# Optimization experiments

Measured on AMD Instinct MI355X. Metric: run time of the kernel, lower is better.

The kernel has to match this reference:

```python
import jax, jax.numpy as jnp
import numpy as np

BS, L, DIM = 16, 2048, 512
NUM_GROUPS, NUM_CODES = 2, 320
CODE_DIM = 256
VAR_DIM = CODE_DIM // NUM_GROUPS  # 128
INNER = DIM * 2                    # projFactor=2
TAU = 2.0                          # max(maxTemp*decay**0, minTemp) at numUpdates=0


def setup_inputs() -> dict:
    key = jax.random.key(0)
    ks = jax.random.split(key, 7)
    x = jax.random.normal(ks[0], (BS, L, DIM), jnp.float32)
    # gumbels = -log(Exp(1)) == standard Gumbel noise, matching torch's exponential_().log().neg()
    gumbels = jax.random.gumbel(ks[1], (BS * L * NUM_GROUPS, NUM_CODES), jnp.float32)
    W1 = jax.random.normal(ks[2], (DIM, INNER), jnp.float32) * (1.0 / np.sqrt(DIM))
    b1 = jnp.zeros((INNER,), jnp.float32)
    W2 = jax.random.normal(ks[3], (INNER, NUM_GROUPS * NUM_CODES), jnp.float32) * (1.0 / np.sqrt(INNER))
    b2 = jnp.zeros((NUM_GROUPS * NUM_CODES,), jnp.float32)
    # nn.init.uniform_ on embeddings: U[0,1); combineGroups=True -> single shared codebook (numCodes, varDim)
    emb = jax.random.uniform(ks[4], (NUM_CODES, VAR_DIM), jnp.float32)
    return {"x": x, "gumbels": gumbels, "W1": W1, "b1": b1, "W2": W2, "b2": b2, "emb": emb}


def reference(x, gumbels, W1, b1, W2, b2, emb):
    bs, l, d = x.shape
    xt = x.reshape(bs * l, d)
    h = jax.nn.gelu(xt @ W1 + b1, approximate=False)          # (N, INNER), torch GELU is exact erf
    logits = (h @ W2 + b2).reshape(bs * l * NUM_GROUPS, NUM_CODES)
    # training path: gumbel-softmax with straight-through hard one-hot
    soft = jax.nn.softmax((logits + gumbels) / TAU, axis=-1)  # (N*G, C)
    idx = jnp.argmax(soft, axis=-1)
    hard = jax.nn.one_hot(idx, NUM_CODES, dtype=soft.dtype)
    st = hard + soft - jax.lax.stop_gradient(soft)            # straight-through estimator
    st = st.reshape(bs * l, NUM_GROUPS, NUM_CODES)
    # combineGroups=True: embeddings repeated per group == shared codebook; the
    # (broadcast-mul).sum(-2) in torch is exactly this contraction (no huge intermediate).
    out = jnp.einsum('ngc,cd->ngd', st, emb)                  # (N, G, varDim)
    return out.reshape(bs, l, NUM_GROUPS * VAR_DIM)
```

## Files before the change

### kernel.cpp

```cpp
#include <hip/hip_runtime.h>
#include <math.h>


#define NTOK   32768
#define DIM    512
#define INNER  1024
#define NC     320
#define NGRP   2
#define VD     128
#define OUTD   256
#define RCAP   2048
#define MARGIN 8.0e-3f

#define L_LIST 16u
#define L_W1T  (64u<<10)
#define L_W2T  (2u<<20)
#define L_XH   (4u<<20)
#define L_H    (36u<<20)
#define L_PART (100u<<20)
#define L_HDW  (104u<<20)
#define WS_NEED (120u<<20)

#define W1F_OFF (1u<<20)
#define W2F_OFF (1u<<21)
#define SMEM_BYTES (65536 + 3328)

typedef _Float16 half8 __attribute__((ext_vector_type(8)));
typedef _Float16 half4 __attribute__((ext_vector_type(4)));
typedef float    f32x4 __attribute__((ext_vector_type(4)));

__device__ __forceinline__ float gelu_f(float s) {
  return 0.5f * s * (1.0f + erff(s * 0.70710678118654752440f));
}

#if defined(__has_builtin) && __has_builtin(__builtin_amdgcn_global_load_lds)
#define GLOAD16(gp, ldsbase, lane) \
  __builtin_amdgcn_global_load_lds((const __attribute__((address_space(1))) void*)(gp), \
                                   (__attribute__((address_space(3))) void*)(ldsbase), 16, 0, 0)
#else
#define GLOAD16(gp, ldsbase, lane) \
  do { *(uint4*)((char*)(ldsbase) + (lane) * 16) = *(const uint4*)(gp); } while (0)
#endif

#define XH_JOBS   2097152
#define W1T_JOBS  65536
#define W2T_JOBS  81920
#define PREP_JOBS (XH_JOBS + W1T_JOBS + W2T_JOBS)
__global__ __launch_bounds__(256)
void prep2_kernel(const float* __restrict__ x, const float* __restrict__ W1,
                  const float* __restrict__ W2, _Float16* __restrict__ xh,
                  _Float16* __restrict__ W1T, _Float16* __restrict__ W2T,
                  unsigned* __restrict__ cnt) {
  const int o = blockIdx.x * 256 + threadIdx.x;
  if (o == 0) cnt[0] = 0u;
  if (o < XH_JOBS) {
    const float4 v0 = *(const float4*)(x + (size_t)o * 8);
    const float4 v1 = *(const float4*)(x + (size_t)o * 8 + 4);
    half8 hv;
    hv[0] = (_Float16)v0.x; hv[1] = (_Float16)v0.y; hv[2] = (_Float16)v0.z; hv[3] = (_Float16)v0.w;
    hv[4] = (_Float16)v1.x; hv[5] = (_Float16)v1.y; hv[6] = (_Float16)v1.z; hv[7] = (_Float16)v1.w;
    *(half8*)(xh + (size_t)o * 8) = hv;
  } else if (o < XH_JOBS + W1T_JOBS) {
    const int q = o - XH_JOBS;
    const int i = q >> 6, k0 = (q & 63) * 8;
#pragma unroll
    for (int j = 0; j < 8; ++j)
      W1T[(size_t)i * DIM + k0 + j] = (_Float16)W1[(size_t)(k0 + j) * INNER + i];
  } else if (o < PREP_JOBS) {
    const int q = o - XH_JOBS - W1T_JOBS;
    const int c = q >> 7, i0 = (q & 127) * 8;
#pragma unroll
    for (int j = 0; j < 8; ++j)
      W2T[(size_t)c * INNER + i0 + j] = (_Float16)W2[(size_t)(i0 + j) * (NC * NGRP) + c];
  }
}

__global__ __launch_bounds__(256, 4)
void gemm1_kernel(const _Float16* __restrict__ xh, const _Float16* __restrict__ W1T,
                  const float* __restrict__ b1, _Float16* __restrict__ h) {
  __shared__ char smem[32768];
  const int tid = threadIdx.x;
  const int w = tid >> 6, l = tid & 63;
  const int l15 = l & 15, lq = l >> 4;
  const int bid = blockIdx.x;
  const int bn = bid & 7, bm = bid >> 3;
  const int wm = w >> 1, wn = w & 1;

  const int r0 = (w * 2 + 0) * 16 + (l >> 2);
  const int r1 = (w * 2 + 1) * 16 + (l >> 2);
  const int c0 = (((l & 3) ^ (r0 & 3)) * 8);
  const int c1 = (((l & 3) ^ (r1 & 3)) * 8);
  const _Float16* gA0 = xh  + (size_t)(bm * 128 + r0) * DIM + c0;
  const _Float16* gA1 = xh  + (size_t)(bm * 128 + r1) * DIM + c1;
  const _Float16* gB0 = W1T + (size_t)(bn * 128 + r0) * DIM + c0;
  const _Float16* gB1 = W1T + (size_t)(bn * 128 + r1) * DIM + c1;
  char* lA0 = smem + (w * 2 + 0) * 1024;
  char* lA1 = smem + (w * 2 + 1) * 1024;
  char* lB0 = smem + 8192 + (w * 2 + 0) * 1024;
  char* lB1 = smem + 8192 + (w * 2 + 1) * 1024;

  f32x4 acc[4][4];
#pragma unroll
  for (int i = 0; i < 4; ++i)
#pragma unroll
    for (int j = 0; j < 4; ++j) { f32x4 z = {0.f, 0.f, 0.f, 0.f}; acc[i][j] = z; }

  const int swz = (lq ^ (l15 & 3)) << 4;
  const int aoff = (wm * 64 + l15) * 64 + swz;
  const int boff = 8192 + (wn * 64 + l15) * 64 + swz;

  for (int ks = 0; ks < 16; ++ks) {
    __syncthreads();
    GLOAD16(gA0 + ks * 32, lA0, l);
    GLOAD16(gA1 + ks * 32, lA1, l);
    GLOAD16(gB0 + ks * 32, lB0, l);
    GLOAD16(gB1 + ks * 32, lB1, l);
    __syncthreads();
    half8 a[4], b[4];
#pragma unroll
    for (int mi = 0; mi < 4; ++mi) a[mi] = *(const half8*)(smem + aoff + mi * 1024);
#pragma unroll
    for (int ni = 0; ni < 4; ++ni) b[ni] = *(const half8*)(smem + boff + ni * 1024);
#pragma unroll
    for (int mi = 0; mi < 4; ++mi)
#pragma unroll
      for (int ni = 0; ni < 4; ++ni)
        acc[mi][ni] = __builtin_amdgcn_mfma_f32_16x16x32_f16(a[mi], b[ni], acc[mi][ni], 0, 0, 0);
  }
  __syncthreads();

  _Float16* eT = (_Float16*)smem;
  float bb[4];
#pragma unroll
  for (int ni = 0; ni < 4; ++ni) bb[ni] = b1[bn * 128 + wn * 64 + ni * 16 + l15];
#pragma unroll
  for (int mi = 0; mi < 4; ++mi) {
    const int row = wm * 64 + mi * 16 + lq * 4;
#pragma unroll
    for (int ni = 0; ni < 4; ++ni) {
      const int col = wn * 64 + ni * 16 + l15;
#pragma unroll
      for (int r = 0; r < 4; ++r)
        eT[(row + r) * 128 + col] = (_Float16)gelu_f(acc[mi][ni][r] + bb[ni]);
    }
  }
  __syncthreads();
#pragma unroll
  for (int it = 0; it < 8; ++it) {
    const int s = tid + it * 256;
    const int row = s >> 4, i8 = s & 15;
    *(half8*)(h + (size_t)(bm * 128 + row) * INNER + bn * 128 + i8 * 8)
        = *(const half8*)(eT + row * 128 + i8 * 8);
  }
}

__global__ __launch_bounds__(256, 4)
void gemm2_kernel(const _Float16* __restrict__ h, const _Float16* __restrict__ W2T,
                  const float* __restrict__ b2, const float* __restrict__ gum,
                  unsigned* __restrict__ part) {
  __shared__ char smem[32768];
  const int tid = threadIdx.x;
  const int w = tid >> 6, l = tid & 63;
  const int l15 = l & 15, lq = l >> 4;
  const int bid = blockIdx.x;
  const int bt = bid % 5, bm = bid / 5;
  const int wm = w >> 1, wn = w & 1;

  const int r0 = (w * 2 + 0) * 16 + (l >> 2);
  const int r1 = (w * 2 + 1) * 16 + (l >> 2);
  const int c0 = (((l & 3) ^ (r0 & 3)) * 8);
  const int c1 = (((l & 3) ^ (r1 & 3)) * 8);
  const _Float16* gA0 = h   + (size_t)(bm * 128 + r0) * INNER + c0;
  const _Float16* gA1 = h   + (size_t)(bm * 128 + r1) * INNER + c1;
  const _Float16* gB0 = W2T + (size_t)(bt * 128 + r0) * INNER + c0;
  const _Float16* gB1 = W2T + (size_t)(bt * 128 + r1) * INNER + c1;
  char* lA0 = smem + (w * 2 + 0) * 1024;
  char* lA1 = smem + (w * 2 + 1) * 1024;
  char* lB0 = smem + 8192 + (w * 2 + 0) * 1024;
  char* lB1 = smem + 8192 + (w * 2 + 1) * 1024;

  f32x4 acc[4][4];
#pragma unroll
  for (int i = 0; i < 4; ++i)
#pragma unroll
    for (int j = 0; j < 4; ++j) { f32x4 z = {0.f, 0.f, 0.f, 0.f}; acc[i][j] = z; }

  const int swz = (lq ^ (l15 & 3)) << 4;
  const int aoff = (wm * 64 + l15) * 64 + swz;
  const int boff = 8192 + (wn * 64 + l15) * 64 + swz;

  for (int ks = 0; ks < 32; ++ks) {
    __syncthreads();
    GLOAD16(gA0 + ks * 32, lA0, l);
    GLOAD16(gA1 + ks * 32, lA1, l);
    GLOAD16(gB0 + ks * 32, lB0, l);
    GLOAD16(gB1 + ks * 32, lB1, l);
    __syncthreads();
    half8 a[4], b[4];
#pragma unroll
    for (int mi = 0; mi < 4; ++mi) a[mi] = *(const half8*)(smem + aoff + mi * 1024);
#pragma unroll
    for (int ni = 0; ni < 4; ++ni) b[ni] = *(const half8*)(smem + boff + ni * 1024);
#pragma unroll
    for (int mi = 0; mi < 4; ++mi)
#pragma unroll
      for (int ni = 0; ni < 4; ++ni)
        acc[mi][ni] = __builtin_amdgcn_mfma_f32_16x16x32_f16(a[mi], b[ni], acc[mi][ni], 0, 0, 0);
  }

  float* eF = (float*)smem;
  const int nm = (bt == 2) ? 8 : 16;
#pragma unroll
  for (int half = 0; half < 2; ++half) {
    __syncthreads();
    if (wm == half) {
#pragma unroll
      for (int mi = 0; mi < 4; ++mi) {
        const int rl = mi * 16 + lq * 4;
#pragma unroll
        for (int ni = 0; ni < 4; ++ni) {
          const int col = wn * 64 + ni * 16 + l15;
#pragma unroll
          for (int r = 0; r < 4; ++r) eF[(rl + r) * 128 + col] = acc[mi][ni][r];
        }
      }
    }
    __syncthreads();
#pragma unroll
    for (int it = 0; it < 8; ++it) {
      const int s = tid + it * 256;
      const int rl = s >> 5, cc = (s & 31) * 4;
      const int t = bm * 128 + half * 64 + rl;
      const float4 lv  = *(const float4*)(eF + rl * 128 + cc);
      const float4 b2v = *(const float4*)(b2 + bt * 128 + cc);
      const float4 gv  = *(const float4*)(gum + (size_t)t * 640 + bt * 128 + cc);
      float m1 = -1e30f, m2 = -1e30f; unsigned i1 = 0;
      const float vv[4] = {(lv.x + b2v.x) + gv.x, (lv.y + b2v.y) + gv.y,
                           (lv.z + b2v.z) + gv.z, (lv.w + b2v.w) + gv.w};
#pragma unroll
      for (int r = 0; r < 4; ++r) {
        const unsigned c = (unsigned)(bt * 128 + cc + r);
        if (vv[r] > m1) { m2 = m1; m1 = vv[r]; i1 = c; }
        else if (vv[r] > m2) m2 = vv[r];
      }
      for (int m = 1; m <= nm; m <<= 1) {
        const float om1 = __shfl_xor(m1, m);
        const float om2 = __shfl_xor(m2, m);
        const unsigned oi = (unsigned)__shfl_xor((int)i1, m);
        const bool take = (om1 > m1) || (om1 == m1 && oi < i1);
        if (take) { m2 = fmaxf(m1, om2); m1 = om1; i1 = oi; }
        else      { m2 = fmaxf(m2, om1); }
      }
      const int lr = tid & 31;
      const bool writer = (bt == 2) ? (lr == 0 || lr == 16) : (lr == 0);
      if (writer) {
        int slot;
        if (bt == 0) slot = 0; else if (bt == 1) slot = 1;
        else if (bt == 3) slot = 4; else if (bt == 4) slot = 5;
        else slot = (i1 < (unsigned)NC) ? 2 : 3;
        const unsigned ing = (i1 < (unsigned)NC) ? i1 : (i1 - NC);
        unsigned* p = part + ((size_t)t * 6 + slot) * 4;
        p[0] = __float_as_uint(m1);
        p[1] = __float_as_uint(m2);
        p[2] = ing;
      }
    }
  }
}

__global__ __launch_bounds__(256, 4)
void reduce_kernel(const unsigned* __restrict__ part, const float* __restrict__ emb,
                   float* __restrict__ out, unsigned* __restrict__ cnt,
                   unsigned* __restrict__ list) {
  __shared__ unsigned idxs[256];
  const int tid = threadIdx.x;
  const int pair = blockIdx.x * 256 + tid;
  const int t = pair >> 1, g = pair & 1;
  float m1 = -1e30f, m2 = -1e30f; unsigned i1 = 0;
#pragma unroll
  for (int s = 0; s < 3; ++s) {
    const unsigned* p = part + ((size_t)t * 6 + g * 3 + s) * 4;
    const float a1 = __uint_as_float(p[0]);
    const float a2 = __uint_as_float(p[1]);
    const unsigned ai = p[2];
    if (a1 > m1) { m2 = fmaxf(m1, a2); m1 = a1; i1 = ai; }
    else         { m2 = fmaxf(m2, a1); }
  }
  idxs[tid] = i1;
  if (m1 - m2 < MARGIN) {
    const unsigned pos = atomicAdd(cnt, 1u);
    if (pos < RCAP) list[pos] = (unsigned)((t << 1) | g);
  }
  __syncthreads();
#pragma unroll
  for (int it = 0; it < 32; ++it) {
    const int s2 = tid + it * 256;
    const int p = s2 >> 5, dd = (s2 & 31) * 4;
    *(float4*)(out + (size_t)blockIdx.x * 32768 + p * 128 + dd)
        = *(const float4*)(emb + (size_t)idxs[p] * VD + dd);
  }
}

__global__ __launch_bounds__(512, 4)
void refine1_kernel(const float* __restrict__ x, const float* __restrict__ W1,
                    const float* __restrict__ b1,
                    const unsigned* __restrict__ cnt, const unsigned* __restrict__ list,
                    float* __restrict__ hdws) {
  __shared__ float xs[DIM];
  unsigned n = cnt[0]; if (n > RCAP) n = RCAP;
  const unsigned e = blockIdx.x;
  if (e >= n) return;
  const unsigned tok = list[e] >> 1;
  const int tid = threadIdx.x;
  xs[tid] = x[(size_t)tok * DIM + tid];
  __syncthreads();
  double a0 = 0.0, a1 = 0.0, c0 = 0.0, c1 = 0.0;
#pragma unroll 4
  for (int k = 0; k < DIM; k += 2) {
    const double x0 = (double)xs[k], x1 = (double)xs[k + 1];
    const float* rr0 = W1 + (size_t)k * INNER + tid;
    const float* rr1 = W1 + (size_t)(k + 1) * INNER + tid;
    a0 += x0 * (double)rr0[0];
    a1 += x0 * (double)rr0[512];
    c0 += x1 * (double)rr1[0];
    c1 += x1 * (double)rr1[512];
  }
  const double s0 = a0 + c0 + (double)b1[tid];
  const double s1 = a1 + c1 + (double)b1[tid + 512];
  hdws[(size_t)e * INNER + tid]       = (float)(0.5 * s0 * (1.0 + erf(s0 * 0.70710678118654752440)));
  hdws[(size_t)e * INNER + tid + 512] = (float)(0.5 * s1 * (1.0 + erf(s1 * 0.70710678118654752440)));
}

__global__ __launch_bounds__(320, 4)
void refine2_kernel(const float* __restrict__ gum, const float* __restrict__ W2,
                    const float* __restrict__ b2, const float* __restrict__ emb,
                    float* __restrict__ out,
                    const unsigned* __restrict__ cnt, const unsigned* __restrict__ list,
                    const float* __restrict__ hdws) {
  __shared__ float hs[INNER];
  __shared__ double wv[5];
  __shared__ int wi[5];
  __shared__ int best;
  unsigned n = cnt[0]; if (n > RCAP) n = RCAP;
  const unsigned e = blockIdx.x;
  if (e >= n) return;
  const unsigned tok = list[e] >> 1;
  const int g = (int)(list[e] & 1u);
  const int tid = threadIdx.x;
  for (int j = tid; j < INNER; j += 320) hs[j] = hdws[(size_t)e * INNER + j];
  __syncthreads();
  const float* w2c = W2 + (size_t)g * NC + tid;
  double acc = 0.0, accb = 0.0;
#pragma unroll 4
  for (int k = 0; k < INNER; k += 2) {
    acc  += (double)hs[k]     * (double)w2c[(size_t)k * (NC * NGRP)];
    accb += (double)hs[k + 1] * (double)w2c[(size_t)(k + 1) * (NC * NGRP)];
  }
  double v = acc + accb + (double)b2[g * NC + tid]
                        + (double)gum[((size_t)tok * 2 + g) * NC + tid];
  int bi = tid;
#pragma unroll
  for (int m = 1; m < 64; m <<= 1) {
    const double ov = __shfl_xor(v, m);
    const int oi = __shfl_xor(bi, m);
    if (ov > v || (ov == v && oi < bi)) { v = ov; bi = oi; }
  }
  if ((tid & 63) == 0) { wv[tid >> 6] = v; wi[tid >> 6] = bi; }
  __syncthreads();
  if (tid == 0) {
    double bv = wv[0]; int bb = wi[0];
#pragma unroll
    for (int k = 1; k < 5; ++k)
      if (wv[k] > bv || (wv[k] == bv && wi[k] < bb)) { bv = wv[k]; bb = wi[k]; }
    best = bb;
  }
  __syncthreads();
  if (tid < VD)
    out[(size_t)tok * OUTD + g * VD + tid] = emb[(size_t)best * VD + tid];
}

#define W1F_N (16 * 64 * 64)
#define W2F_N (32 * 40 * 64)
__global__ void prep_kernel(const float* __restrict__ W1, const float* __restrict__ W2,
                            _Float16* __restrict__ W1F, _Float16* __restrict__ W2F,
                            unsigned* __restrict__ cnt) {
  const int o = blockIdx.x * 256 + threadIdx.x;
  if (o == 0) cnt[0] = 0u;
  if (o < W1F_N) {
    const int l = o & 63, ib = (o >> 6) & 63, ks = o >> 12;
    const int inner = ib * 16 + (l & 15);
    const int kb = ks * 32 + (l >> 4) * 8;
    _Float16* d = W1F + (size_t)o * 8;
#pragma unroll
    for (int j = 0; j < 8; ++j) d[j] = (_Float16)W1[(size_t)(kb + j) * INNER + inner];
  } else {
    const int o2 = o - W1F_N;
    if (o2 < W2F_N) {
      const int l = o2 & 63, cb = (o2 >> 6) % 40, ks = o2 / (40 * 64);
      const int code = cb * 16 + (l & 15);
      const int kb = ks * 32 + (l >> 4) * 8;
      _Float16* d = W2F + (size_t)o2 * 8;
#pragma unroll
      for (int j = 0; j < 8; ++j) d[j] = (_Float16)W2[(size_t)(kb + j) * (NC * NGRP) + code];
    }
  }
}

__global__ __launch_bounds__(512, 4)
void fused_kernel(const float* __restrict__ x, const float* __restrict__ gum,
                  const _Float16* __restrict__ W1F, const _Float16* __restrict__ W2F,
                  const float* __restrict__ b1, const float* __restrict__ b2,
                  const float* __restrict__ emb, float* __restrict__ out,
                  unsigned* __restrict__ cnt, unsigned* __restrict__ list) {
  extern __shared__ char smem[];
  float*    redm1 = (float*)(smem + 65536);
  float*    redm2 = (float*)(smem + 65536 + 1024);
  unsigned* redi  = (unsigned*)(smem + 65536 + 2048);
  unsigned* idxs  = (unsigned*)(smem + 65536 + 3072);
  const int tid = threadIdx.x;
  const int w = tid >> 6, l = tid & 63;
  const int l15 = l & 15, lq = l >> 4;
  const int T0 = blockIdx.x << 5;
#pragma unroll
  for (int i = 0; i < 8; ++i) {
    const int q = tid + i * 512;
    const int row = q >> 7;
    const int c = (q & 127) << 2;
    const float4 v = *(const float4*)(x + (size_t)(T0 + row) * DIM + c);
    half4 hv; hv[0] = (_Float16)v.x; hv[1] = (_Float16)v.y;
    hv[2] = (_Float16)v.z; hv[3] = (_Float16)v.w;
    const unsigned byte = ((unsigned)(row * 1024 + c * 2)) ^ ((unsigned)(row & 7) << 4);
    *(half4*)(smem + byte) = hv;
  }
  __syncthreads();
  {
    f32x4 acc[8][2];
#pragma unroll
    for (int i = 0; i < 8; ++i)
#pragma unroll
      for (int j = 0; j < 2; ++j) { f32x4 z = {0.f,0.f,0.f,0.f}; acc[i][j] = z; }
    const _Float16* w1f = W1F + (size_t)(w * 8) * 512 + (size_t)l * 8;
    for (int ks = 0; ks < 16; ++ks) {
      const int k0 = ks * 32;
      half8 a[8], bf[2];
#pragma unroll
      for (int mt = 0; mt < 8; ++mt) a[mt] = *(const half8*)(w1f + (size_t)(ks * 64 + mt) * 512);
#pragma unroll
      for (int nt = 0; nt < 2; ++nt) {
        const int token = nt * 16 + l15;
        const unsigned byte = ((unsigned)(token * 1024 + (k0 + lq * 8) * 2))
                              ^ ((unsigned)(token & 7) << 4);
        bf[nt] = *(const half8*)(smem + byte);
      }
#pragma unroll
      for (int mt = 0; mt < 8; ++mt)
#pragma unroll
        for (int nt = 0; nt < 2; ++nt)
          acc[mt][nt] = __builtin_amdgcn_mfma_f32_16x16x32_f16(a[mt], bf[nt], acc[mt][nt], 0, 0, 0);
    }
    __syncthreads();
#pragma unroll
    for (int mt = 0; mt < 8; ++mt) {
      const int inner0 = w * 128 + mt * 16 + lq * 4;
      const float4 bv = *(const float4*)(b1 + inner0);
#pragma unroll
      for (int nt = 0; nt < 2; ++nt) {
        const int token = nt * 16 + l15;
        const f32x4 v = acc[mt][nt];
        half4 hv;
        hv[0] = (_Float16)gelu_f(v[0] + bv.x);
        hv[1] = (_Float16)gelu_f(v[1] + bv.y);
        hv[2] = (_Float16)gelu_f(v[2] + bv.z);
        hv[3] = (_Float16)gelu_f(v[3] + bv.w);
        const unsigned byte = ((unsigned)(token * 2048 + inner0 * 2))
                              ^ ((unsigned)(token & 7) << 4);
        *(half4*)(smem + byte) = hv;
      }
    }
  }
  __syncthreads();
  const int g = w >> 2;
  {
    f32x4 acc[5][2];
#pragma unroll
    for (int i = 0; i < 5; ++i)
#pragma unroll
      for (int j = 0; j < 2; ++j) { f32x4 z = {0.f,0.f,0.f,0.f}; acc[i][j] = z; }
    const _Float16* w2f = W2F + (size_t)(w * 5) * 512 + (size_t)l * 8;
    for (int ks = 0; ks < 32; ++ks) {
      const int k0 = ks * 32;
      half8 a[5], bf[2];
#pragma unroll
      for (int mt = 0; mt < 5; ++mt) a[mt] = *(const half8*)(w2f + (size_t)(ks * 40 + mt) * 512);
#pragma unroll
      for (int nt = 0; nt < 2; ++nt) {
        const int token = nt * 16 + l15;
        const unsigned byte = ((unsigned)(token * 2048 + (k0 + lq * 8) * 2))
                              ^ ((unsigned)(token & 7) << 4);
        bf[nt] = *(const half8*)(smem + byte);
      }
#pragma unroll
      for (int mt = 0; mt < 5; ++mt)
#pragma unroll
        for (int nt = 0; nt < 2; ++nt)
          acc[mt][nt] = __builtin_amdgcn_mfma_f32_16x16x32_f16(a[mt], bf[nt], acc[mt][nt], 0, 0, 0);
    }
    float m1v[2] = {-1e30f,-1e30f};
    float m2v[2] = {-1e30f,-1e30f};
    unsigned i1v[2] = {0,0};
#pragma unroll
    for (int mt = 0; mt < 5; ++mt) {
      const int code0 = w * 80 + mt * 16 + lq * 4;
      const int cg0 = code0 - g * NC;
      const float4 b2v = *(const float4*)(b2 + code0);
#pragma unroll
      for (int nt = 0; nt < 2; ++nt) {
        const int tokg = T0 + nt * 16 + l15;
        const float4 gv = *(const float4*)(gum + ((size_t)tokg * 2 + g) * NC + cg0);
        const f32x4 v = acc[mt][nt];
        const float ss[4] = {v[0] + b2v.x + gv.x, v[1] + b2v.y + gv.y,
                             v[2] + b2v.z + gv.z, v[3] + b2v.w + gv.w};
#pragma unroll
        for (int r = 0; r < 4; ++r) {
          const float sv = ss[r];
          const unsigned cc = (unsigned)(cg0 + r);
          if (sv > m1v[nt]) { m2v[nt] = m1v[nt]; m1v[nt] = sv; i1v[nt] = cc; }
          else if (sv > m2v[nt]) m2v[nt] = sv;
        }
      }
    }
#pragma unroll
    for (int mask = 16; mask <= 32; mask <<= 1) {
#pragma unroll
      for (int nt = 0; nt < 2; ++nt) {
        const float om1 = __shfl_xor(m1v[nt], mask);
        const float om2 = __shfl_xor(m2v[nt], mask);
        const unsigned oi = (unsigned)__shfl_xor((int)i1v[nt], mask);
        const bool take = (om1 > m1v[nt]) || (om1 == m1v[nt] && oi < i1v[nt]);
        if (take) { m2v[nt] = fmaxf(m1v[nt], om2); m1v[nt] = om1; i1v[nt] = oi; }
        else      { m2v[nt] = fmaxf(m2v[nt], om1); }
      }
    }
    if (l < 16) {
#pragma unroll
      for (int nt = 0; nt < 2; ++nt) {
        const int tok = nt * 16 + l15;
        redm1[w * 32 + tok] = m1v[nt];
        redm2[w * 32 + tok] = m2v[nt];
        redi [w * 32 + tok] = i1v[nt];
      }
    }
  }
  __syncthreads();
  if (tid < 64) {
    const int pg = tid >> 5;
    const int tok = tid & 31;
    float m1 = -1e30f, m2 = -1e30f; unsigned i1 = 0;
#pragma unroll
    for (int k = 0; k < 4; ++k) {
      const int ww = pg * 4 + k;
      const float a1 = redm1[ww * 32 + tok];
      const float a2 = redm2[ww * 32 + tok];
      const unsigned ai = redi[ww * 32 + tok];
      if (a1 > m1) { m2 = fmaxf(m1, a2); m1 = a1; i1 = ai; }
      else         { m2 = fmaxf(m2, a1); }
    }
    idxs[tid] = i1;
    if (m1 - m2 < MARGIN) {
      const unsigned pos = atomicAdd(cnt, 1u);
      if (pos < RCAP) list[pos] = (unsigned)(((T0 + tok) << 1) | pg);
    }
  }
  __syncthreads();
#pragma unroll
  for (int i = 0; i < 4; ++i) {
    const int q = tid + i * 512;
    const int p = q >> 5;
    const int dd = q & 31;
    const int pg = p >> 5;
    const int tok = p & 31;
    const unsigned idx = idxs[p];
    *(float4*)(out + (size_t)(T0 + tok) * OUTD + pg * VD + dd * 4)
      = *(const float4*)(emb + (size_t)idx * VD + dd * 4);
  }
}

__global__ __launch_bounds__(512, 1)
void refine_kernel(const float* __restrict__ x, const float* __restrict__ gum,
                   const float* __restrict__ W1, const float* __restrict__ b1,
                   const float* __restrict__ W2, const float* __restrict__ b2,
                   const float* __restrict__ emb, float* __restrict__ out,
                   const unsigned* __restrict__ cnt, const unsigned* __restrict__ list) {
  __shared__ double xs[4][DIM];
  __shared__ double hd[4][INNER];
  __shared__ double sc[4][NC];
  __shared__ int amax[4];
  const int tid = threadIdx.x;
  unsigned n = cnt[0];
  if (n > RCAP) n = RCAP;
  for (unsigned base = blockIdx.x * 4u; base < n; base += gridDim.x * 4u) {
    const int nb = (int)((n - base) < 4u ? (n - base) : 4u);
    unsigned ng[4];
#pragma unroll
    for (int e = 0; e < 4; ++e) ng[e] = list[base + (e < nb ? e : 0)];
    for (int e = 0; e < nb; ++e)
      xs[e][tid] = (double)x[(size_t)(ng[e] >> 1) * DIM + tid];
    __syncthreads();
#pragma unroll
    for (int jj = 0; jj < 2; ++jj) {
      const int j = tid + jj * 512;
      double a0 = 0, a1 = 0, a2 = 0, a3 = 0;
      for (int k = 0; k < DIM; ++k) {
        const double wvv = (double)W1[(size_t)k * INNER + j];
        a0 += xs[0][k] * wvv; a1 += xs[1][k] * wvv;
        a2 += xs[2][k] * wvv; a3 += xs[3][k] * wvv;
      }
      const double bb = (double)b1[j];
      const double s0 = a0 + bb, s1 = a1 + bb, s2 = a2 + bb, s3 = a3 + bb;
      hd[0][j] = 0.5 * s0 * (1.0 + erf(s0 * 0.70710678118654752440));
      hd[1][j] = 0.5 * s1 * (1.0 + erf(s1 * 0.70710678118654752440));
      hd[2][j] = 0.5 * s2 * (1.0 + erf(s2 * 0.70710678118654752440));
      hd[3][j] = 0.5 * s3 * (1.0 + erf(s3 * 0.70710678118654752440));
    }
    __syncthreads();
    for (int task = tid; task < 4 * NC; task += 512) {
      const int e = task / NC;
      const int c = task - e * NC;
      if (e < nb) {
        const unsigned tok = ng[e] >> 1;
        const int gg = (int)(ng[e] & 1u);
        const float* w2c = W2 + (size_t)gg * NC + c;
        double acc = 0.0;
        for (int k = 0; k < INNER; ++k)
          acc += hd[e][k] * (double)w2c[(size_t)k * (NC * NGRP)];
        sc[e][c] = acc + (double)b2[gg * NC + c]
                       + (double)gum[((size_t)tok * 2 + gg) * NC + c];
      }
    }
    __syncthreads();
    if (tid < 4 && tid < nb) {
      double bestv = sc[tid][0]; int bi = 0;
      for (int c = 1; c < NC; ++c)
        if (sc[tid][c] > bestv) { bestv = sc[tid][c]; bi = c; }
      amax[tid] = bi;
    }
    __syncthreads();
    {
      const int e = tid >> 7;
      const int d = tid & 127;
      if (e < nb) {
        const unsigned tok = ng[e] >> 1;
        const int gg = (int)(ng[e] & 1u);
        out[(size_t)tok * OUTD + gg * VD + d] = emb[(size_t)amax[e] * VD + d];
      }
    }
    __syncthreads();
  }
}

extern "C" void kernel_launch(void* const* d_in, const int* in_sizes, int n_in,
                              void* d_out, int out_size, void* d_ws, size_t ws_size,
                              hipStream_t stream) {
  (void)in_sizes; (void)n_in; (void)out_size;
  const float* x   = (const float*)d_in[0];
  const float* gum = (const float*)d_in[1];
  const float* W1  = (const float*)d_in[2];
  const float* b1  = (const float*)d_in[3];
  const float* W2  = (const float*)d_in[4];
  const float* b2  = (const float*)d_in[5];
  const float* emb = (const float*)d_in[6];
  float* out = (float*)d_out;
  char* ws = (char*)d_ws;
  unsigned* cnt  = (unsigned*)ws;
  unsigned* list = (unsigned*)(ws + L_LIST);

  if (ws_size >= (size_t)WS_NEED) {
    _Float16* W1T = (_Float16*)(ws + L_W1T);
    _Float16* W2T = (_Float16*)(ws + L_W2T);
    _Float16* xh  = (_Float16*)(ws + L_XH);
    _Float16* h   = (_Float16*)(ws + L_H);
    unsigned* part = (unsigned*)(ws + L_PART);
    float* hdws = (float*)(ws + L_HDW);

    prep2_kernel<<<(PREP_JOBS + 255) / 256, 256, 0, stream>>>(x, W1, W2, xh, W1T, W2T, cnt);
    gemm1_kernel<<<(NTOK / 128) * 8, 256, 0, stream>>>(xh, W1T, b1, h);
    gemm2_kernel<<<(NTOK / 128) * 5, 256, 0, stream>>>(h, W2T, b2, gum, part);
    reduce_kernel<<<NTOK * NGRP / 256, 256, 0, stream>>>(part, emb, out, cnt, list);
    refine1_kernel<<<RCAP, 512, 0, stream>>>(x, W1, b1, cnt, list, hdws);
    refine2_kernel<<<RCAP, 320, 0, stream>>>(gum, W2, b2, emb, out, cnt, list, hdws);
  } else {
    _Float16* W1F = (_Float16*)(ws + W1F_OFF);
    _Float16* W2F = (_Float16*)(ws + W2F_OFF);
    hipFuncSetAttribute((const void*)fused_kernel,
                        hipFuncAttributeMaxDynamicSharedMemorySize, SMEM_BYTES);
    const int prep_items = W1F_N + W2F_N;
    prep_kernel<<<(prep_items + 255) / 256, 256, 0, stream>>>(W1, W2, W1F, W2F, cnt);
    fused_kernel<<<NTOK / 32, 512, SMEM_BYTES, stream>>>(x, gum, W1F, W2F, b1, b2,
                                                         emb, out, cnt, list);
    refine_kernel<<<256, 512, 0, stream>>>(x, gum, W1, b1, W2, b2, emb, out, cnt, list);
  }
}
```

Before: 334.5 us.

## Double-buffer LDS staging in GEMM kernels, remap blocks per XCD, swizzle epilogue LDS

Both GEMM kernels now prefetch the next K-slice into a second 16KB LDS buffer while computing on the current one, replacing two barriers per iteration with one. Block indices are remapped so consecutive blocks on the same XCD share row tiles, which should improve L2 locality. The epilogue LDS writes and reads are XOR-swizzled to reduce bank conflicts. The smem array is still declared as 32KB, which now holds both buffers exactly. It is unclear from the visible code whether these GEMM kernels or the fused kernel further down are the ones launched.

```diff
diff --git a/kernel.cpp b/kernel.cpp
--- a/kernel.cpp
+++ b/kernel.cpp
@@ -34,12 +34,12 @@
 }
 
 #if defined(__has_builtin) && __has_builtin(__builtin_amdgcn_global_load_lds)
-#define GLOAD16(gp, ldsbase, lane) \
+#define GLOAD16(gp, ldsbase) \
   __builtin_amdgcn_global_load_lds((const __attribute__((address_space(1))) void*)(gp), \
                                    (__attribute__((address_space(3))) void*)(ldsbase), 16, 0, 0)
 #else
-#define GLOAD16(gp, ldsbase, lane) \
-  do { *(uint4*)((char*)(ldsbase) + (lane) * 16) = *(const uint4*)(gp); } while (0)
+#define GLOAD16(gp, ldsbase) \
+  do { *(uint4*)((char*)(ldsbase) + (threadIdx.x & 63) * 16) = *(const uint4*)(gp); } while (0)
 #endif
 
 #define XH_JOBS   2097152
@@ -83,7 +83,8 @@
   const int w = tid >> 6, l = tid & 63;
   const int l15 = l & 15, lq = l >> 4;
   const int bid = blockIdx.x;
-  const int bn = bid & 7, bm = bid >> 3;
+  const int xcd = bid & 7, j = bid >> 3;
+  const int bm = xcd * 32 + (j >> 3), bn = j & 7;
   const int wm = w >> 1, wn = w & 1;
 
   const int r0 = (w * 2 + 0) * 16 + (l >> 2);
@@ -94,40 +95,43 @@
   const _Float16* gA1 = xh  + (size_t)(bm * 128 + r1) * DIM + c1;
   const _Float16* gB0 = W1T + (size_t)(bn * 128 + r0) * DIM + c0;
   const _Float16* gB1 = W1T + (size_t)(bn * 128 + r1) * DIM + c1;
-  char* lA0 = smem + (w * 2 + 0) * 1024;
-  char* lA1 = smem + (w * 2 + 1) * 1024;
-  char* lB0 = smem + 8192 + (w * 2 + 0) * 1024;
-  char* lB1 = smem + 8192 + (w * 2 + 1) * 1024;
+
+#define STAGE_G(buf, ks) do { \
+    char* b_ = smem + (buf) * 16384; \
+    GLOAD16(gA0 + (ks) * 32, b_ + (w * 2 + 0) * 1024); \
+    GLOAD16(gA1 + (ks) * 32, b_ + (w * 2 + 1) * 1024); \
+    GLOAD16(gB0 + (ks) * 32, b_ + 8192 + (w * 2 + 0) * 1024); \
+    GLOAD16(gB1 + (ks) * 32, b_ + 8192 + (w * 2 + 1) * 1024); \
+  } while (0)
 
   f32x4 acc[4][4];
 #pragma unroll
   for (int i = 0; i < 4; ++i)
 #pragma unroll
-    for (int j = 0; j < 4; ++j) { f32x4 z = {0.f, 0.f, 0.f, 0.f}; acc[i][j] = z; }
+    for (int jj = 0; jj < 4; ++jj) { f32x4 z = {0.f, 0.f, 0.f, 0.f}; acc[i][jj] = z; }
 
   const int swz = (lq ^ (l15 & 3)) << 4;
   const int aoff = (wm * 64 + l15) * 64 + swz;
   const int boff = 8192 + (wn * 64 + l15) * 64 + swz;
 
+  STAGE_G(0, 0);
+  __syncthreads();
   for (int ks = 0; ks < 16; ++ks) {
-    __syncthreads();
-    GLOAD16(gA0 + ks * 32, lA0, l);
-    GLOAD16(gA1 + ks * 32, lA1, l);
-    GLOAD16(gB0 + ks * 32, lB0, l);
-    GLOAD16(gB1 + ks * 32, lB1, l);
-    __syncthreads();
+    const int cur = ks & 1;
+    if (ks + 1 < 16) STAGE_G(cur ^ 1, ks + 1);
+    const char* base = smem + cur * 16384;
     half8 a[4], b[4];
 #pragma unroll
-    for (int mi = 0; mi < 4; ++mi) a[mi] = *(const half8*)(smem + aoff + mi * 1024);
-#pragma unroll
-    for (int ni = 0; ni < 4; ++ni) b[ni] = *(const half8*)(smem + boff + ni * 1024);
+    for (int mi = 0; mi < 4; ++mi) a[mi] = *(const half8*)(base + aoff + mi * 1024);
+#pragma unroll
+    for (int ni = 0; ni < 4; ++ni) b[ni] = *(const half8*)(base + boff + ni * 1024);
 #pragma unroll
     for (int mi = 0; mi < 4; ++mi)
 #pragma unroll
       for (int ni = 0; ni < 4; ++ni)
         acc[mi][ni] = __builtin_amdgcn_mfma_f32_16x16x32_f16(a[mi], b[ni], acc[mi][ni], 0, 0, 0);
-  }
-  __syncthreads();
+    __syncthreads();
+  }
 
   _Float16* eT = (_Float16*)smem;
   float bb[4];
@@ -138,7 +142,7 @@
     const int row = wm * 64 + mi * 16 + lq * 4;
 #pragma unroll
     for (int ni = 0; ni < 4; ++ni) {
-      const int col = wn * 64 + ni * 16 + l15;
+      const int col = (wn * 64 + ni * 16 + l15) ^ (lq << 4);
 #pragma unroll
       for (int r = 0; r < 4; ++r)
         eT[(row + r) * 128 + col] = (_Float16)gelu_f(acc[mi][ni][r] + bb[ni]);
@@ -149,8 +153,9 @@
   for (int it = 0; it < 8; ++it) {
     const int s = tid + it * 256;
     const int row = s >> 4, i8 = s & 15;
+    const int colp = (i8 * 8) ^ (((row >> 2) & 3) << 4);
     *(half8*)(h + (size_t)(bm * 128 + row) * INNER + bn * 128 + i8 * 8)
-        = *(const half8*)(eT + row * 128 + i8 * 8);
+        = *(const half8*)(eT + row * 128 + colp);
   }
 }
 
@@ -163,7 +168,8 @@
   const int w = tid >> 6, l = tid & 63;
   const int l15 = l & 15, lq = l >> 4;
   const int bid = blockIdx.x;
-  const int bt = bid % 5, bm = bid / 5;
+  const int xcd = bid & 7, j = bid >> 3;
+  const int bm = xcd * 32 + j / 5, bt = j % 5;
   const int wm = w >> 1, wn = w & 1;
 
   const int r0 = (w * 2 + 0) * 16 + (l >> 2);
@@ -174,38 +180,34 @@
   const _Float16* gA1 = h   + (size_t)(bm * 128 + r1) * INNER + c1;
   const _Float16* gB0 = W2T + (size_t)(bt * 128 + r0) * INNER + c0;
   const _Float16* gB1 = W2T + (size_t)(bt * 128 + r1) * INNER + c1;
-  char* lA0 = smem + (w * 2 + 0) * 1024;
-  char* lA1 = smem + (w * 2 + 1) * 1024;
-  char* lB0 = smem + 8192 + (w * 2 + 0) * 1024;
-  char* lB1 = smem + 8192 + (w * 2 + 1) * 1024;
 
   f32x4 acc[4][4];
 #pragma unroll
   for (int i = 0; i < 4; ++i)
 #pragma unroll
-    for (int j = 0; j < 4; ++j) { f32x4 z = {0.f, 0.f, 0.f, 0.f}; acc[i][j] = z; }
+    for (int jj = 0; jj < 4; ++jj) { f32x4 z = {0.f, 0.f, 0.f, 0.f}; acc[i][jj] = z; }
 
   const int swz = (lq ^ (l15 & 3)) << 4;
   const int aoff = (wm * 64 + l15) * 64 + swz;
   const int boff = 8192 + (wn * 64 + l15) * 64 + swz;
 
+  STAGE_G(0, 0);
+  __syncthreads();
   for (int ks = 0; ks < 32; ++ks) {
-    __syncthreads();
-    GLOAD16(gA0 + ks * 32, lA0, l);
-    GLOAD16(gA1 + ks * 32, lA1, l);
-    GLOAD16(gB0 + ks * 32, lB0, l);
-    GLOAD16(gB1 + ks * 32, lB1, l);
-    __syncthreads();
+    const int cur = ks & 1;
+    if (ks + 1 < 32) STAGE_G(cur ^ 1, ks + 1);
+    const char* base = smem + cur * 16384;
     half8 a[4], b[4];
 #pragma unroll
-    for (int mi = 0; mi < 4; ++mi) a[mi] = *(const half8*)(smem + aoff + mi * 1024);
-#pragma unroll
-    for (int ni = 0; ni < 4; ++ni) b[ni] = *(const half8*)(smem + boff + ni * 1024);
+    for (int mi = 0; mi < 4; ++mi) a[mi] = *(const half8*)(base + aoff + mi * 1024);
+#pragma unroll
+    for (int ni = 0; ni < 4; ++ni) b[ni] = *(const half8*)(base + boff + ni * 1024);
 #pragma unroll
     for (int mi = 0; mi < 4; ++mi)
 #pragma unroll
       for (int ni = 0; ni < 4; ++ni)
         acc[mi][ni] = __builtin_amdgcn_mfma_f32_16x16x32_f16(a[mi], b[ni], acc[mi][ni], 0, 0, 0);
+    __syncthreads();
   }
 
   float* eF = (float*)smem;
@@ -219,7 +221,7 @@
         const int rl = mi * 16 + lq * 4;
 #pragma unroll
         for (int ni = 0; ni < 4; ++ni) {
-          const int col = wn * 64 + ni * 16 + l15;
+          const int col = (wn * 64 + ni * 16 + l15) ^ ((lq & 1) << 4);
 #pragma unroll
           for (int r = 0; r < 4; ++r) eF[(rl + r) * 128 + col] = acc[mi][ni][r];
         }
@@ -230,8 +232,9 @@
     for (int it = 0; it < 8; ++it) {
       const int s = tid + it * 256;
       const int rl = s >> 5, cc = (s & 31) * 4;
+      const int ccp = cc ^ (((rl >> 2) & 1) << 4);
       const int t = bm * 128 + half * 64 + rl;
-      const float4 lv  = *(const float4*)(eF + rl * 128 + cc);
+      const float4 lv  = *(const float4*)(eF + rl * 128 + ccp);
       const float4 b2v = *(const float4*)(b2 + bt * 128 + cc);
       const float4 gv  = *(const float4*)(gum + (size_t)t * 640 + bt * 128 + cc);
       float m1 = -1e30f, m2 = -1e30f; unsigned i1 = 0;
@@ -438,7 +441,7 @@
 #pragma unroll
     for (int i = 0; i < 8; ++i)
 #pragma unroll
-      for (int j = 0; j < 2; ++j) { f32x4 z = {0.f,0.f,0.f,0.f}; acc[i][j] = z; }
+      for (int jj = 0; jj < 2; ++jj) { f32x4 z = {0.f,0.f,0.f,0.f}; acc[i][jj] = z; }
     const _Float16* w1f = W1F + (size_t)(w * 8) * 512 + (size_t)l * 8;
     for (int ks = 0; ks < 16; ++ks) {
       const int k0 = ks * 32;
@@ -485,7 +488,7 @@
 #pragma unroll
     for (int i = 0; i < 5; ++i)
 #pragma unroll
-      for (int j = 0; j < 2; ++j) { f32x4 z = {0.f,0.f,0.f,0.f}; acc[i][j] = z; }
+      for (int jj = 0; jj < 2; ++jj) { f32x4 z = {0.f,0.f,0.f,0.f}; acc[i][jj] = z; }
     const _Float16* w2f = W2F + (size_t)(w * 5) * 512 + (size_t)l * 8;
     for (int ks = 0; ks < 32; ++ks) {
       const int k0 = ks * 32;
```

Result: faster. 314.1 us (-6.1%).
